# Performance work log

Measured on AMD Instinct MI355X. Metric: run time of the kernel, lower is better.

## Reference

```python
import jax, jax.numpy as jnp
import numpy as np

K = 5          # kernel_size
PAD = (K - 1) // 2  # fixed_padding with dilation=1, stride=1 -> 'same'


def setup_inputs() -> dict:
    key = jax.random.key(0)
    kx, kw = jax.random.split(key)
    x = jax.random.normal(kx, (4, 8, 512, 512), dtype=jnp.float32)
    # nn.Parameter initialized to zeros in the original; use small random values
    # so the op is non-trivial (math is identical for any weight values).
    weight = jax.random.normal(kw, (8, 8, K, K), dtype=jnp.float32) * 0.05
    return {"x": x, "weight": weight}


def reference(x, weight):
    """Morphological dilation2d with hard max (soft_max=False).

    out[n,o,h,w] = max_{c,dy,dx} ( x_pad[n,c,h+dy,w+dx] + weight[o,c,dy,dx] )
    Faithful to: pad zeros -> unfold -> weight + x -> max over dim C*k*k.
    Computed as a fused sliding-window max-plus reduction (no (N,C,k,k,H,W)
    unfold tensor is materialized; loop is over the fixed k*k kernel taps).
    """
    N, C, H, W = x.shape
    O = weight.shape[0]
    xp = jnp.pad(x, ((0, 0), (0, 0), (PAD, PAD), (PAD, PAD)))  # zero pad, as in F.pad
    out = jnp.full((N, O, H, W), -jnp.inf, dtype=x.dtype)
    for dy in range(K):
        for dx in range(K):
            patch = xp[:, :, dy:dy + H, dx:dx + W]           # (N,C,H,W)
            w_tap = weight[:, :, dy, dx]                      # (O,C)
            # (N,1,C,H,W) + (1,O,C,1,1) -> max over C -> (N,O,H,W)
            term = patch[:, None] + w_tap[None, :, :, None, None]
            out = jnp.maximum(out, jnp.max(term, axis=2))
    return out
```

## Files before the change

kernel.cpp:

```cpp
#include <hip/hip_runtime.h>
#include <math.h>
#include <stdint.h>

#define KK 5
#define PADK 2
#define C_IN 8
#define O_OUT 8
#define HH 512
#define WW 512
#define TH 8
#define TW 128
#define CH 4
#define LROWS 12
#define LCOLS 136
#define WSTR 12
#define NW (O_OUT * C_IN * KK * KK)
#define XHALF (CH * LROWS * (LCOLS / 2))

static __device__ __forceinline__ float max3f(float a, float b, float c) {
    float d;
    asm("v_max3_f32 %0, %1, %2, %3" : "=v"(d) : "v"(a), "v"(b), "v"(c));
    return d;
}

__global__ __launch_bounds__(512, 8)
void dil_kernel(const float* __restrict__ x,
                const float* __restrict__ wf,
                float* __restrict__ out) {
    __shared__ __align__(16) float xlds[CH][LROWS][LCOLS];
    __shared__ __align__(16) float wlds[C_IN * 4 * KK * WSTR];

    const int tid = threadIdx.x;
    const int w0 = blockIdx.x * TW;
    const int h0 = blockIdx.y * TH;
    const int n  = blockIdx.z;
    const float* xn = x + (size_t)n * (C_IN * HH * WW);

    const int l   = tid & 63;
    const int wid = tid >> 6;
    const int og  = wid & 3;
    const int rbase = (wid >> 2) * 4;

    const float* xbase = &xlds[0][rbase][2 * l];
    const float* wog   = wlds + og * (KK * WSTR);

    float acc[2][4][2];
    #pragma unroll
    for (int a = 0; a < 2; ++a)
        #pragma unroll
        for (int j = 0; j < 4; ++j) {
            acc[a][j][0] = -INFINITY;
            acc[a][j][1] = -INFINITY;
        }

    for (int h = 0; h < 2; ++h) {
        if (h) __syncthreads();

        for (int idx = tid; idx < XHALF; idx += 512) {
            int cc  = idx / (LROWS * (LCOLS / 2));
            int rem = idx - cc * (LROWS * (LCOLS / 2));
            int r   = rem / (LCOLS / 2);
            int jp  = rem - r * (LCOLS / 2);
            int gh = h0 - PADK + r;
            int gw = w0 - PADK + 2 * jp;
            float v0 = 0.f, v1 = 0.f;
            if ((unsigned)gh < (unsigned)HH) {
                const float* row = xn + ((size_t)(h * CH + cc) * HH + gh) * WW;
                if ((unsigned)gw < (unsigned)WW) v0 = row[gw];
                if ((unsigned)(gw + 1) < (unsigned)WW) v1 = row[gw + 1];
            }
            *(float2*)&xlds[cc][r][2 * jp] = make_float2(v0, v1);
        }
        if (h == 0) {
            for (int t = tid; t < NW; t += 512) {
                int dx = t % KK;  int q = t / KK;
                int o2 = q & 1;   q >>= 1;
                int dy = q % KK;  q /= KK;
                int g  = q & 3;   int c = q >> 2;
                int o = g * 2 + o2;
                wlds[((c * 4 + g) * KK + dy) * WSTR + o2 * KK + dx] =
                    wf[((o * C_IN + c) * KK + dy) * KK + dx];
            }
        }
        __syncthreads();

        const float* wh = wog + h * (CH * 4 * KK * WSTR);

        #pragma unroll
        for (int cc = 0; cc < CH; ++cc) {
            #pragma unroll
            for (int dy = 0; dy < KK; ++dy) {
                const float* wch = wh + (cc * 4 * KK + dy) * WSTR;
                float4 wa = *(const float4*)(wch);
                float4 wv = *(const float4*)(wch + 4);
                float2 wc2 = *(const float2*)(wch + 8);
                const float w[10] = {wa.x, wa.y, wa.z, wa.w,
                                     wv.x, wv.y, wv.z, wv.w, wc2.x, wc2.y};
                #pragma unroll
                for (int j = 0; j < 4; ++j) {
                    const float* lr = xbase + cc * (LROWS * LCOLS)
                                            + (dy + j) * LCOLS;
                    float2 A = *(const float2*)(lr);
                    float2 B = *(const float2*)(lr + 2);
                    float2 D = *(const float2*)(lr + 4);
                    const float u0 = A.x, u1 = A.y, u2 = B.x,
                                u3 = B.y, u4 = D.x, u5 = D.y;
                    #pragma unroll
                    for (int o2 = 0; o2 < 2; ++o2) {
                        const float* wo = &w[o2 * 5];
                        float t0 = u0 + wo[0], t1 = u1 + wo[1],
                              t2 = u2 + wo[2], t3 = u3 + wo[3],
                              t4 = u4 + wo[4];
                        acc[o2][j][0] = max3f(acc[o2][j][0],
                                              max3f(t0, t1, t2),
                                              fmaxf(t3, t4));
                        float s0 = u1 + wo[0], s1 = u2 + wo[1],
                              s2 = u3 + wo[2], s3 = u4 + wo[3],
                              s4 = u5 + wo[4];
                        acc[o2][j][1] = max3f(acc[o2][j][1],
                                              max3f(s0, s1, s2),
                                              fmaxf(s3, s4));
                    }
                }
            }
        }
    }

    float* onp = out + (size_t)n * (O_OUT * HH * WW);
    const int hB = h0 + rbase;
    const int wcol = w0 + 2 * l;
    float* obase = &onp[((size_t)(og * 2) * HH + hB) * WW + wcol];
    #pragma unroll
    for (int o2 = 0; o2 < 2; ++o2) {
        #pragma unroll
        for (int j = 0; j < 4; ++j) {
            float2 rr = make_float2(acc[o2][j][0], acc[o2][j][1]);
            *(float2*)(obase + (size_t)o2 * (HH * WW) + j * WW) = rr;
        }
    }
}

extern "C" void kernel_launch(void* const* d_in, const int* in_sizes, int n_in,
                              void* d_out, int out_size, void* d_ws, size_t ws_size,
                              hipStream_t stream) {
    const float* x   = (const float*)d_in[0];
    const float* wgt = (const float*)d_in[1];
    float* out = (float*)d_out;

    dim3 grid(WW / TW, HH / TH, 4);
    dim3 block(512);
    dil_kernel<<<grid, block, 0, stream>>>(x, wgt, out);
}
```

Measured before the change: 65.11 us.

## Prefetch second channel half into registers while computing first half

Global loads of the input tile now go into a per-thread register staging array, and are written to LDS in a separate step. The loads for the second channel half are issued before computing the first half, so their global latency overlaps with that compute. The loads also become branch-free float2 reads with clamped addresses, and masking is applied at store time. This costs 14 extra VGPRs per thread and one extra barrier, which may lower occupancy under the 512x8 launch bounds.

```diff
diff --git a/kernel.cpp b/kernel.cpp
--- a/kernel.cpp
+++ b/kernel.cpp
@@ -16,6 +16,8 @@
 #define WSTR 12
 #define NW (O_OUT * C_IN * KK * KK)
 #define XHALF (CH * LROWS * (LCOLS / 2))
+#define NSTG 7
+#define XPAD (NSTG * 512)
 
 static __device__ __forceinline__ float max3f(float a, float b, float c) {
     float d;
@@ -27,7 +29,7 @@
 void dil_kernel(const float* __restrict__ x,
                 const float* __restrict__ wf,
                 float* __restrict__ out) {
-    __shared__ __align__(16) float xlds[CH][LROWS][LCOLS];
+    __shared__ __align__(16) float xlds[2 * XPAD];
     __shared__ __align__(16) float wlds[C_IN * 4 * KK * WSTR];
 
     const int tid = threadIdx.x;
@@ -41,8 +43,41 @@
     const int og  = wid & 3;
     const int rbase = (wid >> 2) * 4;
 
-    const float* xbase = &xlds[0][rbase][2 * l];
-    const float* wog   = wlds + og * (KK * WSTR);
+    float2 stg[NSTG];
+
+#define STAGE_L(hh)                                                        \
+    _Pragma("unroll")                                                      \
+    for (int k = 0; k < NSTG; ++k) {                                       \
+        int idx = tid + k * 512;                                           \
+        int ci  = min(idx, XHALF - 1);                                     \
+        int cc  = ci / (LROWS * (LCOLS / 2));                              \
+        int rem = ci - cc * (LROWS * (LCOLS / 2));                         \
+        int r   = rem / (LCOLS / 2);                                       \
+        int jp  = rem - r * (LCOLS / 2);                                   \
+        int gh  = min(max(h0 - PADK + r, 0), HH - 1);                      \
+        int gw  = min(max(w0 - PADK + 2 * jp, 0), WW - 2);                 \
+        stg[k] = *(const float2*)(                                         \
+            xn + ((size_t)((hh) * CH + cc) * HH + gh) * WW + gw);          \
+    }
+
+#define STAGE_W()                                                          \
+    _Pragma("unroll")                                                      \
+    for (int k = 0; k < NSTG; ++k) {                                       \
+        int idx = tid + k * 512;                                           \
+        int ci  = min(idx, XHALF - 1);                                     \
+        int cc  = ci / (LROWS * (LCOLS / 2));                              \
+        int rem = ci - cc * (LROWS * (LCOLS / 2));                         \
+        int r   = rem / (LCOLS / 2);                                       \
+        int jp  = rem - r * (LCOLS / 2);                                   \
+        int gh  = h0 - PADK + r;                                           \
+        int gw  = w0 - PADK + 2 * jp;                                      \
+        bool ok = ((unsigned)gh < (unsigned)HH) &                          \
+                  ((unsigned)gw < (unsigned)WW) & (idx < XHALF);           \
+        float2 v;                                                          \
+        v.x = ok ? stg[k].x : 0.f;                                         \
+        v.y = ok ? stg[k].y : 0.f;                                         \
+        *(float2*)(&xlds[2 * idx]) = v;                                    \
+    }
 
     float acc[2][4][2];
     #pragma unroll
@@ -53,78 +88,73 @@
             acc[a][j][1] = -INFINITY;
         }
 
-    for (int h = 0; h < 2; ++h) {
-        if (h) __syncthreads();
+    const float* xbase = &xlds[rbase * LCOLS + 2 * l];
+    const float* wog   = wlds + og * (KK * WSTR);
 
-        for (int idx = tid; idx < XHALF; idx += 512) {
-            int cc  = idx / (LROWS * (LCOLS / 2));
-            int rem = idx - cc * (LROWS * (LCOLS / 2));
-            int r   = rem / (LCOLS / 2);
-            int jp  = rem - r * (LCOLS / 2);
-            int gh = h0 - PADK + r;
-            int gw = w0 - PADK + 2 * jp;
-            float v0 = 0.f, v1 = 0.f;
-            if ((unsigned)gh < (unsigned)HH) {
-                const float* row = xn + ((size_t)(h * CH + cc) * HH + gh) * WW;
-                if ((unsigned)gw < (unsigned)WW) v0 = row[gw];
-                if ((unsigned)(gw + 1) < (unsigned)WW) v1 = row[gw + 1];
-            }
-            *(float2*)&xlds[cc][r][2 * jp] = make_float2(v0, v1);
-        }
-        if (h == 0) {
-            for (int t = tid; t < NW; t += 512) {
-                int dx = t % KK;  int q = t / KK;
-                int o2 = q & 1;   q >>= 1;
-                int dy = q % KK;  q /= KK;
-                int g  = q & 3;   int c = q >> 2;
-                int o = g * 2 + o2;
-                wlds[((c * 4 + g) * KK + dy) * WSTR + o2 * KK + dx] =
-                    wf[((o * C_IN + c) * KK + dy) * KK + dx];
-            }
-        }
-        __syncthreads();
+#define COMPUTE(hh)                                                        \
+    _Pragma("unroll")                                                      \
+    for (int cc = 0; cc < CH; ++cc) {                                      \
+        _Pragma("unroll")                                                  \
+        for (int dy = 0; dy < KK; ++dy) {                                  \
+            const float* wch = wog + ((hh) * CH * 4 * KK                   \
+                                      + cc * 4 * KK + dy) * WSTR;          \
+            float4 wa = *(const float4*)(wch);                             \
+            float4 wv = *(const float4*)(wch + 4);                         \
+            float2 wc2 = *(const float2*)(wch + 8);                        \
+            const float w[10] = {wa.x, wa.y, wa.z, wa.w,                   \
+                                 wv.x, wv.y, wv.z, wv.w, wc2.x, wc2.y};    \
+            _Pragma("unroll")                                              \
+            for (int j = 0; j < 4; ++j) {                                  \
+                const float* lr = xbase + cc * (LROWS * LCOLS)             \
+                                        + (dy + j) * LCOLS;                \
+                float2 A = *(const float2*)(lr);                           \
+                float2 B = *(const float2*)(lr + 2);                       \
+                float2 D = *(const float2*)(lr + 4);                       \
+                const float u0 = A.x, u1 = A.y, u2 = B.x,                  \
+                            u3 = B.y, u4 = D.x, u5 = D.y;                  \
+                _Pragma("unroll")                                          \
+                for (int o2 = 0; o2 < 2; ++o2) {                           \
+                    const float* wo = &w[o2 * 5];                          \
+                    float t0 = u0 + wo[0], t1 = u1 + wo[1],                \
+                          t2 = u2 + wo[2], t3 = u3 + wo[3],                \
+                          t4 = u4 + wo[4];                                 \
+                    acc[o2][j][0] = max3f(acc[o2][j][0],                   \
+                                          max3f(t0, t1, t2),               \
+                                          fmaxf(t3, t4));                  \
+                    float s0 = u1 + wo[0], s1 = u2 + wo[1],                \
+                          s2 = u3 + wo[2], s3 = u4 + wo[3],                \
+                          s4 = u5 + wo[4];                                 \
+                    acc[o2][j][1] = max3f(acc[o2][j][1],                   \
+                                          max3f(s0, s1, s2),               \
+                                          fmaxf(s3, s4));                  \
+                }                                                          \
+            }                                                              \
+        }                                                                  \
+    }
 
-        const float* wh = wog + h * (CH * 4 * KK * WSTR);
+    STAGE_L(0)
+    for (int t = tid; t < NW; t += 512) {
+        int dx = t % KK;  int q = t / KK;
+        int o2 = q & 1;   q >>= 1;
+        int dy = q % KK;  q /= KK;
+        int g  = q & 3;   int c = q >> 2;
+        int o = g * 2 + o2;
+        wlds[((c * 4 + g) * KK + dy) * WSTR + o2 * KK + dx] =
+            wf[((o * C_IN + c) * KK + dy) * KK + dx];
+    }
+    STAGE_W()
+    __syncthreads();
 
-        #pragma unroll
-        for (int cc = 0; cc < CH; ++cc) {
-            #pragma unroll
-            for (int dy = 0; dy < KK; ++dy) {
-                const float* wch = wh + (cc * 4 * KK + dy) * WSTR;
-                float4 wa = *(const float4*)(wch);
-                float4 wv = *(const float4*)(wch + 4);
-                float2 wc2 = *(const float2*)(wch + 8);
-                const float w[10] = {wa.x, wa.y, wa.z, wa.w,
-                                     wv.x, wv.y, wv.z, wv.w, wc2.x, wc2.y};
-                #pragma unroll
-                for (int j = 0; j < 4; ++j) {
-                    const float* lr = xbase + cc * (LROWS * LCOLS)
-                                            + (dy + j) * LCOLS;
-                    float2 A = *(const float2*)(lr);
-                    float2 B = *(const float2*)(lr + 2);
-                    float2 D = *(const float2*)(lr + 4);
-                    const float u0 = A.x, u1 = A.y, u2 = B.x,
-                                u3 = B.y, u4 = D.x, u5 = D.y;
-                    #pragma unroll
-                    for (int o2 = 0; o2 < 2; ++o2) {
-                        const float* wo = &w[o2 * 5];
-                        float t0 = u0 + wo[0], t1 = u1 + wo[1],
-                              t2 = u2 + wo[2], t3 = u3 + wo[3],
-                              t4 = u4 + wo[4];
-                        acc[o2][j][0] = max3f(acc[o2][j][0],
-                                              max3f(t0, t1, t2),
-                                              fmaxf(t3, t4));
-                        float s0 = u1 + wo[0], s1 = u2 + wo[1],
-                              s2 = u3 + wo[2], s3 = u4 + wo[3],
-                              s4 = u5 + wo[4];
-                        acc[o2][j][1] = max3f(acc[o2][j][1],
-                                              max3f(s0, s1, s2),
-                                              fmaxf(s3, s4));
-                    }
-                }
-            }
-        }
-    }
+    STAGE_L(1)
+    COMPUTE(0)
+    __syncthreads();
+    STAGE_W()
+    __syncthreads();
+    COMPUTE(1)
+
+#undef STAGE_L
+#undef STAGE_W
+#undef COMPUTE
 
     float* onp = out + (size_t)n * (O_OUT * HH * WW);
     const int hB = h0 + rbase;
```

Measured after the change: 82.34 us. +26.5%, slower.
